# Kernel optimization log

Measured on AMD Instinct MI355X. Metric: run time of the kernel, lower is better.

The kernel has to match this reference:

```python
import jax, jax.numpy as jnp
import numpy as np

HID, NH, NKV, HD = 2048, 16, 8, 128
EPS = 1e-6
THETA = 10000.0
SCALE = HD ** -0.5


def setup_inputs() -> dict:
    key = jax.random.key(0)
    ks = jax.random.split(key, 6)
    S = 2048
    return {
        "positions": jnp.arange(S, dtype=jnp.int32),
        "hidden_states": jax.random.normal(ks[0], (S, HID), dtype=jnp.float32),
        "layernorm_weight": jax.random.uniform(ks[1], (HID,), dtype=jnp.float32, minval=0.5, maxval=1.5),
        "w_qkv": jax.random.normal(ks[2], ((NH + 2 * NKV) * HD, HID), dtype=jnp.float32) * 0.02,
        "w_o": jax.random.normal(ks[3], (HID, NH * HD), dtype=jnp.float32) * 0.02,
        "q_norm_w": jax.random.uniform(ks[4], (HD,), dtype=jnp.float32, minval=0.5, maxval=1.5),
        "k_norm_w": jax.random.uniform(ks[5], (HD,), dtype=jnp.float32, minval=0.5, maxval=1.5),
    }


def _rmsnorm(x, w, eps=EPS):
    var = jnp.mean(jnp.square(x), axis=-1, keepdims=True)
    return x * jax.lax.rsqrt(var + eps) * w


def _rope(x, cos, sin):
    # x: [S, h, HD]; cos/sin: [S, 1, HD//2] (neox-style rotate-half)
    x1, x2 = x[..., : HD // 2], x[..., HD // 2 :]
    return jnp.concatenate([x1 * cos - x2 * sin, x2 * cos + x1 * sin], axis=-1)


def reference(positions, hidden_states, layernorm_weight, w_qkv, w_o, q_norm_w, k_norm_w):
    S = hidden_states.shape[0]
    # Fused RMSNorm + QKV projection
    hn = _rmsnorm(hidden_states, layernorm_weight)
    qkv = hn @ w_qkv.T  # [S, (NH+2*NKV)*HD]
    q, k, v = jnp.split(qkv, [NH * HD, (NH + NKV) * HD], axis=-1)
    q = q.reshape(S, NH, HD)
    k = k.reshape(S, NKV, HD)
    v = v.reshape(S, NKV, HD)
    # Per-head QK RMSNorm
    q = _rmsnorm(q, q_norm_w)
    k = _rmsnorm(k, k_norm_w)
    # RoPE
    inv_freq = 1.0 / (THETA ** (jnp.arange(0, HD, 2, dtype=jnp.float32) / HD))
    freqs = positions.astype(jnp.float32)[:, None] * inv_freq  # [S, HD//2]
    cos = jnp.cos(freqs)[:, None, :]
    sin = jnp.sin(freqs)[:, None, :]
    q = _rope(q, cos, sin)
    k = _rope(k, cos, sin)
    # GQA: expand kv heads to match query heads
    rep = NH // NKV
    k = jnp.repeat(k, rep, axis=1)  # [S, NH, HD]
    v = jnp.repeat(v, rep, axis=1)
    # Causal attention
    scores = jnp.einsum("shd,thd->hst", q, k) * SCALE  # [NH, S, S]
    causal = jnp.tril(jnp.ones((S, S), dtype=bool))
    scores = jnp.where(causal, scores, jnp.finfo(scores.dtype).min)
    probs = jax.nn.softmax(scores, axis=-1)
    out = jnp.einsum("hst,thd->shd", probs, v)  # [S, NH, HD]
    # Output projection
    return out.reshape(S, NH * HD) @ w_o.T
```

## Files before the change

kernel.cpp:

```cpp
#include <hip/hip_runtime.h>
#include <hip/hip_bf16.h>
#include <math.h>

#define HID 2048
#define NH 16
#define NKV 8
#define HD 128
#define SEQ 2048
#define EPS 1e-6f
#define SCALE 0.08838834764831845f

typedef __attribute__((ext_vector_type(8))) short bf8_t;
typedef __attribute__((ext_vector_type(4))) float f4_t;

__device__ __forceinline__ short f2bf(float f) {
    union { __hip_bfloat16 h; short s; } u;
    u.h = __float2bfloat16(f);
    return u.s;
}
__device__ __forceinline__ float bf2f(short s) {
    union { short s; __hip_bfloat16 h; } u;
    u.s = s;
    return __bfloat162float(u.h);
}
__device__ __forceinline__ bf8_t pack8(const float4& a, const float4& b) {
    bf8_t r;
    r[0] = f2bf(a.x); r[1] = f2bf(a.y); r[2] = f2bf(a.z); r[3] = f2bf(a.w);
    r[4] = f2bf(b.x); r[5] = f2bf(b.y); r[6] = f2bf(b.z); r[7] = f2bf(b.w);
    return r;
}
__device__ __forceinline__ void gload16(const short* g, short* l) {
    __builtin_amdgcn_global_load_lds(
        (const __attribute__((address_space(1))) unsigned int*)g,
        (__attribute__((address_space(3))) unsigned int*)l, 16, 0, 0);
}

__device__ __forceinline__ float wave_reduce_sum(float v) {
#pragma unroll
    for (int off = 32; off > 0; off >>= 1) v += __shfl_xor(v, off);
    return v;
}

__global__ __launch_bounds__(256) void prep_kernel(
    const float* __restrict__ w_qkv, short* __restrict__ wqb,
    const float* __restrict__ w_o, short* __restrict__ wob,
    const float* __restrict__ x, const float* __restrict__ w,
    short* __restrict__ out) {
    int bid = blockIdx.x;
    int tid = threadIdx.x;
    if (bid < 4096) {
        int i = bid * 256 + tid;
        float4 a = *(const float4*)(w_qkv + (size_t)i * 8);
        float4 b = *(const float4*)(w_qkv + (size_t)i * 8 + 4);
        *(bf8_t*)(wqb + (size_t)i * 8) = pack8(a, b);
        return;
    }
    if (bid < 6144) {
        int i = (bid - 4096) * 256 + tid;
        float4 a = *(const float4*)(w_o + (size_t)i * 8);
        float4 b = *(const float4*)(w_o + (size_t)i * 8 + 4);
        *(bf8_t*)(wob + (size_t)i * 8) = pack8(a, b);
        return;
    }
    int row = bid - 6144;
    const float* xr = x + (size_t)row * HID;
    float4 a = *(const float4*)(xr + tid * 8);
    float4 b = *(const float4*)(xr + tid * 8 + 4);
    float ss = a.x * a.x + a.y * a.y + a.z * a.z + a.w * a.w +
               b.x * b.x + b.y * b.y + b.z * b.z + b.w * b.w;
    ss = wave_reduce_sum(ss);
    __shared__ float part[4];
    __shared__ float s_scale;
    if ((tid & 63) == 0) part[tid >> 6] = ss;
    __syncthreads();
    if (tid == 0) {
        float t = part[0] + part[1] + part[2] + part[3];
        s_scale = rsqrtf(t / (float)HID + EPS);
    }
    __syncthreads();
    float sc = s_scale;
    float4 wa = *(const float4*)(w + tid * 8);
    float4 wb = *(const float4*)(w + tid * 8 + 4);
    float4 oa = make_float4(a.x * sc * wa.x, a.y * sc * wa.y,
                            a.z * sc * wa.z, a.w * sc * wa.w);
    float4 ob = make_float4(b.x * sc * wb.x, b.y * sc * wb.y,
                            b.z * sc * wb.z, b.w * sc * wb.w);
    *(bf8_t*)(out + (size_t)row * HID + tid * 8) = pack8(oa, ob);
}

template <int MODE>
__global__ __launch_bounds__(256) void gemm_mfma_kernel(
    const short* __restrict__ A, const short* __restrict__ B,
    float* __restrict__ Cf, short* __restrict__ Q, short* __restrict__ Kp,
    short* __restrict__ Vr, int M, int N, int K) {
    __shared__ short As[128][64];
    __shared__ short Bs[128][64];
    int tid = threadIdx.x;
    int wv = tid >> 6, lane = tid & 63;
    int n16 = lane & 15, qd = lane >> 4;
    int m0 = blockIdx.y * 128, n0 = blockIdx.x * 128;
    int wm = (wv >> 1) * 64, wn = (wv & 1) * 64;
    int sr8 = lane >> 3, slot = lane & 7;

    size_t ainv[4], binv[4];
#pragma unroll
    for (int it = 0; it < 4; ++it) {
        int row = wv * 32 + it * 8 + sr8;
        int chunk = (slot - row) & 7;
        ainv[it] = (size_t)(m0 + row) * K + chunk * 8;
        binv[it] = (size_t)(n0 + row) * K + chunk * 8;
    }

    f4_t acc[4][4];
#pragma unroll
    for (int i = 0; i < 4; ++i)
#pragma unroll
        for (int j = 0; j < 4; ++j) acc[i][j] = (f4_t){0.f, 0.f, 0.f, 0.f};

    for (int k0 = 0; k0 < K; k0 += 64) {
        __syncthreads();
#pragma unroll
        for (int it = 0; it < 4; ++it) {
            gload16(A + ainv[it] + k0, &As[wv * 32 + it * 8][0]);
            gload16(B + binv[it] + k0, &Bs[wv * 32 + it * 8][0]);
        }
        __syncthreads();

        bf8_t af[4][2], bf[4][2];
#pragma unroll
        for (int t = 0; t < 4; ++t)
#pragma unroll
            for (int ks = 0; ks < 2; ++ks) {
                int ar = wm + t * 16 + n16;
                af[t][ks] = *(const bf8_t*)&As[ar][(((ks * 4 + qd) + ar) & 7) * 8];
                int br = wn + t * 16 + n16;
                bf[t][ks] = *(const bf8_t*)&Bs[br][(((ks * 4 + qd) + br) & 7) * 8];
            }
#pragma unroll
        for (int ks = 0; ks < 2; ++ks)
#pragma unroll
            for (int mt = 0; mt < 4; ++mt)
#pragma unroll
                for (int nt = 0; nt < 4; ++nt)
                    acc[mt][nt] = __builtin_amdgcn_mfma_f32_16x16x32_bf16(
                        af[mt][ks], bf[nt][ks], acc[mt][nt], 0, 0, 0);
    }

#pragma unroll
    for (int mt = 0; mt < 4; ++mt)
#pragma unroll
        for (int nt = 0; nt < 4; ++nt)
#pragma unroll
            for (int r = 0; r < 4; ++r) {
                int gm = m0 + wm + mt * 16 + qd * 4 + r;
                int gn = n0 + wn + nt * 16 + n16;
                float v = acc[mt][nt][r];
                if (MODE == 0) {
                    Cf[(size_t)gm * N + gn] = v;
                } else {
                    if (gn < NH * HD)
                        Q[(size_t)gm * (NH * HD) + gn] = f2bf(v);
                    else if (gn < (NH + NKV) * HD)
                        Kp[(size_t)gm * (NKV * HD) + (gn - NH * HD)] = f2bf(v);
                    else
                        Vr[(size_t)gm * (NKV * HD) + (gn - (NH + NKV) * HD)] = f2bf(v);
                }
            }
}

__global__ __launch_bounds__(256) void mid_kernel(
    const short* __restrict__ vr, short* __restrict__ vt,
    short* __restrict__ q, short* __restrict__ k,
    const float* __restrict__ qw, const float* __restrict__ kw,
    const int* __restrict__ pos) {
    int bid = blockIdx.x;
    int tid = threadIdx.x;
    if (bid < 512) {
        __shared__ short t[64][64];
        int s0 = (bid & 31) * 64, d0 = (bid >> 5) * 64;
        int sl = tid >> 3, ch = tid & 7;
#pragma unroll
        for (int it = 0; it < 2; ++it) {
            int s_local = it * 32 + sl;
            bf8_t vv = *(const bf8_t*)(vr + (size_t)(s0 + s_local) * (NKV * HD) + d0 + ch * 8);
            *(bf8_t*)&t[s_local][((ch + s_local) & 7) * 8] = vv;
        }
        __syncthreads();
#pragma unroll
        for (int it = 0; it < 2; ++it) {
            int d_local = it * 32 + sl;
            int sbase = ch * 8;
            bf8_t o;
#pragma unroll
            for (int j = 0; j < 8; ++j) {
                int s = sbase + j;
                o[j] = t[s][(((d_local >> 3) + s) & 7) * 8 + (d_local & 7)];
            }
            *(bf8_t*)(vt + (size_t)(d0 + d_local) * SEQ + s0 + sbase) = o;
        }
        return;
    }
    int u = (bid - 512) * 2 + (tid >> 7);
    int ui = tid >> 7, d = tid & 127;
    int s = u / 24, hh = u % 24;
    short* ptr;
    const float* w;
    if (hh < NH) {
        ptr = q + (size_t)s * (NH * HD) + hh * HD;
        w = qw;
    } else {
        ptr = k + (size_t)s * (NKV * HD) + (hh - NH) * HD;
        w = kw;
    }
    float x = bf2f(ptr[d]);
    float ss = wave_reduce_sum(x * x);
    __shared__ float part[2][2];
    if ((d & 63) == 0) part[ui][d >> 6] = ss;
    __syncthreads();
    float tot = part[ui][0] + part[ui][1];
    float xn = x * rsqrtf(tot / (float)HD + EPS) * w[d];
    __shared__ float sh[2][HD];
    sh[ui][d] = xn;
    __syncthreads();
    int j = d & 63;
    float inv = __expf((float)j * -0.14391156831f);
    float fr = (float)pos[s] * inv;
    float sn, cs;
    __sincosf(fr, &sn, &cs);
    float o;
    if (d < 64)
        o = xn * cs - sh[ui][d + 64] * sn;
    else
        o = xn * cs + sh[ui][d - 64] * sn;
    ptr[d] = f2bf(o);
}

__device__ __forceinline__ void attn_stage(
    short (&kb)[64][128], short (&vb)[128][64],
    const short* __restrict__ kg, const short* __restrict__ vg,
    int t0, const int (&kinv)[4], const int (&vinv)[4], int wv) {
#pragma unroll
    for (int it = 0; it < 4; ++it) {
        gload16(kg + (size_t)t0 * (NKV * HD) + kinv[it], &kb[wv * 16 + it * 4][0]);
        gload16(vg + t0 + vinv[it], &vb[wv * 32 + it * 8][0]);
    }
}

__device__ __forceinline__ void attn_tile(
    const short (&kb)[64][128], const short (&vb)[128][64],
    short (&psh)[4][2][16][64],
    const bf8_t (&qf)[2][4], f4_t (&of)[2][8],
    float (&m_i)[2][4], float (&l_p)[2][4],
    int wv, int n, int qd, int koff) {
    f4_t sc[2][4];
#pragma unroll
    for (int g = 0; g < 2; ++g)
#pragma unroll
        for (int kk = 0; kk < 4; ++kk) sc[g][kk] = (f4_t){0.f, 0.f, 0.f, 0.f};
#pragma unroll
    for (int kk = 0; kk < 4; ++kk) {
        int key = kk * 16 + n;
#pragma unroll
        for (int ks = 0; ks < 4; ++ks) {
            bf8_t kf = *(const bf8_t*)&kb[key][(((ks * 4 + qd) + key) & 15) * 8];
            sc[0][kk] = __builtin_amdgcn_mfma_f32_16x16x32_bf16(qf[0][ks], kf, sc[0][kk], 0, 0, 0);
            sc[1][kk] = __builtin_amdgcn_mfma_f32_16x16x32_bf16(qf[1][ks], kf, sc[1][kk], 0, 0, 0);
        }
    }
#pragma unroll
    for (int g = 0; g < 2; ++g) {
        int rows0 = wv * 32 + g * 16;
        bool needm = (koff + 63 > rows0);
#pragma unroll
        for (int kk = 0; kk < 4; ++kk)
#pragma unroll
            for (int r = 0; r < 4; ++r) {
                float s = sc[g][kk][r] * SCALE;
                if (needm && (koff + kk * 16 + n > rows0 + qd * 4 + r)) s = -1e30f;
                sc[g][kk][r] = s;
            }
#pragma unroll
        for (int r = 0; r < 4; ++r) {
            float mx = fmaxf(fmaxf(sc[g][0][r], sc[g][1][r]),
                             fmaxf(sc[g][2][r], sc[g][3][r]));
#pragma unroll
            for (int off = 1; off < 16; off <<= 1) mx = fmaxf(mx, __shfl_xor(mx, off));
            float mnew = fmaxf(m_i[g][r], mx);
            float al = __expf(m_i[g][r] - mnew);
            m_i[g][r] = mnew;
            float lsum = 0.f;
            int row = qd * 4 + r;
#pragma unroll
            for (int kk = 0; kk < 4; ++kk) {
                float p = __expf(sc[g][kk][r] - mnew);
                psh[wv][g][row][((kk * 16 + n) + row * 8) & 63] = f2bf(p);
                lsum += p;
            }
            l_p[g][r] = l_p[g][r] * al + lsum;
#pragma unroll
            for (int nb = 0; nb < 8; ++nb) of[g][nb][r] *= al;
        }
    }
    __builtin_amdgcn_wave_barrier();
#pragma unroll
    for (int ks2 = 0; ks2 < 2; ++ks2) {
        bf8_t pf0 = *(const bf8_t*)&psh[wv][0][n][((ks2 * 32 + qd * 8) + n * 8) & 63];
        bf8_t pf1 = *(const bf8_t*)&psh[wv][1][n][((ks2 * 32 + qd * 8) + n * 8) & 63];
#pragma unroll
        for (int nb = 0; nb < 8; ++nb) {
            int dim = nb * 16 + n;
            bf8_t vf = *(const bf8_t*)&vb[dim][(((ks2 * 4 + qd) + dim) & 7) * 8];
            of[0][nb] = __builtin_amdgcn_mfma_f32_16x16x32_bf16(pf0, vf, of[0][nb], 0, 0, 0);
            of[1][nb] = __builtin_amdgcn_mfma_f32_16x16x32_bf16(pf1, vf, of[1][nb], 0, 0, 0);
        }
    }
}

__global__ __launch_bounds__(256, 2) void attn_chunk_kernel(
    const short* __restrict__ q, const short* __restrict__ k,
    const short* __restrict__ vt, short* __restrict__ opart,
    float* __restrict__ ml) {
    __shared__ short kbufA[64][128], kbufB[64][128];
    __shared__ short vbufA[128][64], vbufB[128][64];
    __shared__ short psh[4][2][16][64];

    int tid = threadIdx.x;
    int wv = tid >> 6, lane = tid & 63;
    int n = lane & 15, qd = lane >> 4;

    int i = blockIdx.x;
    int hs = i >> 8, p = i & 255;
    int h = p >> 4;
    int qt = hs ? (p & 15) : (15 - (p & 15));
    int c = hs;
    int qbase = qt * 128;
    int tstart = c ? (qt + 1) : 0;
    int tcount = qt + 1;
    int kvh = h >> 1;

    int kinv[4], vinv[4];
#pragma unroll
    for (int it = 0; it < 4; ++it) {
        int key = wv * 16 + it * 4 + (lane >> 4);
        int ck = ((lane & 15) - key) & 15;
        kinv[it] = key * (NKV * HD) + kvh * HD + ck * 8;
        int dim = wv * 32 + it * 8 + (lane >> 3);
        int cv = ((lane & 7) - dim) & 7;
        vinv[it] = (kvh * HD + dim) * SEQ + cv * 8;
    }

    bf8_t qf[2][4];
#pragma unroll
    for (int g = 0; g < 2; ++g) {
        const short* qp =
            q + (size_t)(qbase + wv * 32 + g * 16 + n) * (NH * HD) + h * HD + qd * 8;
#pragma unroll
        for (int ks = 0; ks < 4; ++ks) qf[g][ks] = *(const bf8_t*)(qp + ks * 32);
    }

    f4_t of[2][8];
#pragma unroll
    for (int g = 0; g < 2; ++g)
#pragma unroll
        for (int x = 0; x < 8; ++x) of[g][x] = (f4_t){0.f, 0.f, 0.f, 0.f};
    float m_i[2][4] = {{-1e30f, -1e30f, -1e30f, -1e30f},
                       {-1e30f, -1e30f, -1e30f, -1e30f}};
    float l_p[2][4] = {{0.f, 0.f, 0.f, 0.f}, {0.f, 0.f, 0.f, 0.f}};

    attn_stage(kbufA, vbufA, k, vt, tstart * 64, kinv, vinv, wv);
    for (int tt = 0; tt < tcount; tt += 2) {
        __syncthreads();
        if (tt + 1 < tcount)
            attn_stage(kbufB, vbufB, k, vt, (tstart + tt + 1) * 64, kinv, vinv, wv);
        attn_tile(kbufA, vbufA, psh, qf, of, m_i, l_p, wv, n, qd,
                  (tstart + tt) * 64 - qbase);
        if (tt + 1 < tcount) {
            __syncthreads();
            if (tt + 2 < tcount)
                attn_stage(kbufA, vbufA, k, vt, (tstart + tt + 2) * 64, kinv, vinv, wv);
            attn_tile(kbufB, vbufB, psh, qf, of, m_i, l_p, wv, n, qd,
                      (tstart + tt + 1) * 64 - qbase);
        }
    }

    float lred[2][4];
#pragma unroll
    for (int g = 0; g < 2; ++g)
#pragma unroll
        for (int r = 0; r < 4; ++r) {
            float l = l_p[g][r];
#pragma unroll
            for (int off = 1; off < 16; off <<= 1) l += __shfl_xor(l, off);
            lred[g][r] = l;
        }

    size_t pb = ((size_t)(h * 16 + qt)) * 2 + c;
    short* op = opart + pb * (128 * 128);
#pragma unroll
    for (int g = 0; g < 2; ++g)
#pragma unroll
        for (int nb = 0; nb < 8; ++nb)
#pragma unroll
            for (int r = 0; r < 4; ++r) {
                int rl = wv * 32 + g * 16 + qd * 4 + r;
                op[rl * 128 + nb * 16 + n] = f2bf(of[g][nb][r]);
            }
    if (n == 0) {
#pragma unroll
        for (int g = 0; g < 2; ++g)
#pragma unroll
            for (int r = 0; r < 4; ++r) {
                int rl = wv * 32 + g * 16 + qd * 4 + r;
                ml[pb * 256 + rl * 2] = m_i[g][r];
                ml[pb * 256 + rl * 2 + 1] = lred[g][r];
            }
    }
}

__global__ __launch_bounds__(256) void attn_merge_kernel(
    const short* __restrict__ opart, const float* __restrict__ ml,
    short* __restrict__ o) {
    int bid = blockIdx.x;
    int h = bid >> 4, qt = bid & 15;
    int tid = threadIdx.x;
    int r = tid >> 1, hf = tid & 1;
    size_t pb0 = ((size_t)(h * 16 + qt)) * 2;
    size_t pb1 = pb0 + 1;
    float m0 = ml[pb0 * 256 + r * 2], l0 = ml[pb0 * 256 + r * 2 + 1];
    float m1 = ml[pb1 * 256 + r * 2], l1 = ml[pb1 * 256 + r * 2 + 1];
    float M = fmaxf(m0, m1);
    float w0 = __expf(m0 - M), w1 = __expf(m1 - M);
    float invL = 1.0f / (w0 * l0 + w1 * l1);
    int row = qt * 128 + r;
#pragma unroll
    for (int j = 0; j < 8; ++j) {
        int d0 = hf * 64 + j * 8;
        bf8_t a = *(const bf8_t*)(opart + pb0 * (128 * 128) + r * 128 + d0);
        bf8_t b = *(const bf8_t*)(opart + pb1 * (128 * 128) + r * 128 + d0);
        bf8_t e;
#pragma unroll
        for (int x = 0; x < 8; ++x)
            e[x] = f2bf((w0 * bf2f(a[x]) + w1 * bf2f(b[x])) * invL);
        *(bf8_t*)(o + (size_t)row * (NH * HD) + h * HD + d0) = e;
    }
}

extern "C" void kernel_launch(void* const* d_in, const int* in_sizes, int n_in,
                              void* d_out, int out_size, void* d_ws, size_t ws_size,
                              hipStream_t stream) {
    const int* positions   = (const int*)d_in[0];
    const float* hidden    = (const float*)d_in[1];
    const float* ln_w      = (const float*)d_in[2];
    const float* w_qkv     = (const float*)d_in[3];
    const float* w_o       = (const float*)d_in[4];
    const float* q_norm_w  = (const float*)d_in[5];
    const float* k_norm_w  = (const float*)d_in[6];
    float* out = (float*)d_out;

    char* base = (char*)d_ws;
    short* hnb   = (short*)(base);
    short* wqb   = (short*)(base + ((size_t)8 << 20));
    short* vtb   = (short*)(base + ((size_t)8 << 20));
    float* mlbuf = (float*)(base + ((size_t)12 << 20));
    short* wob   = (short*)(base + ((size_t)24 << 20));
    short* qbf   = (short*)(base + ((size_t)32 << 20));
    short* kbf   = (short*)(base + ((size_t)40 << 20));
    short* vrow  = (short*)(base + ((size_t)44 << 20));
    short* opart = (short*)d_out;

    prep_kernel<<<8192, 256, 0, stream>>>(w_qkv, wqb, w_o, wob, hidden, ln_w, hnb);
    gemm_mfma_kernel<1><<<dim3(32, 16), 256, 0, stream>>>(
        hnb, wqb, nullptr, qbf, kbf, vrow, SEQ, (NH + 2 * NKV) * HD, HID);
    mid_kernel<<<512 + 24576, 256, 0, stream>>>(
        vrow, vtb, qbf, kbf, q_norm_w, k_norm_w, positions);
    attn_chunk_kernel<<<512, 256, 0, stream>>>(qbf, kbf, vtb, opart, mlbuf);
    attn_merge_kernel<<<256, 256, 0, stream>>>(opart, mlbuf, hnb);
    gemm_mfma_kernel<0><<<dim3(16, 16), 256, 0, stream>>>(
        hnb, wob, out, nullptr, nullptr, nullptr, SEQ, NH * HD, HID);
}
```

Baseline: 279.3 us.

## Split attention into fixed six-tile KV chunks with variable-count merge

Attention work is now partitioned into chunks of at most six 64-key tiles per query tile, giving 816 blocks instead of 512 two-way splits, and the merge kernel combines a variable number of partials. Shared memory drops from double-buffered K/V to single buffers and the P staging buffer is halved so three blocks fit per CU. The goal is better load balance and occupancy across the causal triangle. In exchange it gives up the prefetch overlap of loads with compute, and it writes and reads more partial outputs in the merge.

```diff
diff --git a/kernel.cpp b/kernel.cpp
--- a/kernel.cpp
+++ b/kernel.cpp
@@ -235,6 +235,15 @@
     ptr[d] = f2bf(o);
 }
 
+__constant__ int c_qtb[17] = {0,1,2,3,5,7,9,12,15,18,22,26,30,35,40,45,51};
+
+__device__ __forceinline__ short* part_ptr(short* opA, short* opB, int pb) {
+    return pb < 512 ? opA + (size_t)pb * 16384 : opB + (size_t)(pb - 512) * 16384;
+}
+__device__ __forceinline__ const short* part_ptrc(const short* opA, const short* opB, int pb) {
+    return pb < 512 ? opA + (size_t)pb * 16384 : opB + (size_t)(pb - 512) * 16384;
+}
+
 __device__ __forceinline__ void attn_stage(
     short (&kb)[64][128], short (&vb)[128][64],
     const short* __restrict__ kg, const short* __restrict__ vg,
@@ -248,7 +257,7 @@
 
 __device__ __forceinline__ void attn_tile(
     const short (&kb)[64][128], const short (&vb)[128][64],
-    short (&psh)[4][2][16][64],
+    short (&psh)[4][16][64],
     const bf8_t (&qf)[2][4], f4_t (&of)[2][8],
     float (&m_i)[2][4], float (&l_p)[2][4],
     int wv, int n, int qd, int koff) {
@@ -267,6 +276,7 @@
             sc[1][kk] = __builtin_amdgcn_mfma_f32_16x16x32_bf16(qf[1][ks], kf, sc[1][kk], 0, 0, 0);
         }
     }
+    bf8_t pf[2][2];
 #pragma unroll
     for (int g = 0; g < 2; ++g) {
         int rows0 = wv * 32 + g * 16;
@@ -293,50 +303,53 @@
 #pragma unroll
             for (int kk = 0; kk < 4; ++kk) {
                 float p = __expf(sc[g][kk][r] - mnew);
-                psh[wv][g][row][((kk * 16 + n) + row * 8) & 63] = f2bf(p);
+                psh[wv][row][((kk * 16 + n) + row * 8) & 63] = f2bf(p);
                 lsum += p;
             }
             l_p[g][r] = l_p[g][r] * al + lsum;
 #pragma unroll
             for (int nb = 0; nb < 8; ++nb) of[g][nb][r] *= al;
         }
-    }
-    __builtin_amdgcn_wave_barrier();
-#pragma unroll
-    for (int ks2 = 0; ks2 < 2; ++ks2) {
-        bf8_t pf0 = *(const bf8_t*)&psh[wv][0][n][((ks2 * 32 + qd * 8) + n * 8) & 63];
-        bf8_t pf1 = *(const bf8_t*)&psh[wv][1][n][((ks2 * 32 + qd * 8) + n * 8) & 63];
+        __builtin_amdgcn_wave_barrier();
+#pragma unroll
+        for (int ks2 = 0; ks2 < 2; ++ks2)
+            pf[g][ks2] = *(const bf8_t*)&psh[wv][n][((ks2 * 32 + qd * 8) + n * 8) & 63];
+        __builtin_amdgcn_wave_barrier();
+    }
+#pragma unroll
+    for (int ks2 = 0; ks2 < 2; ++ks2)
 #pragma unroll
         for (int nb = 0; nb < 8; ++nb) {
             int dim = nb * 16 + n;
             bf8_t vf = *(const bf8_t*)&vb[dim][(((ks2 * 4 + qd) + dim) & 7) * 8];
-            of[0][nb] = __builtin_amdgcn_mfma_f32_16x16x32_bf16(pf0, vf, of[0][nb], 0, 0, 0);
-            of[1][nb] = __builtin_amdgcn_mfma_f32_16x16x32_bf16(pf1, vf, of[1][nb], 0, 0, 0);
-        }
-    }
-}
-
-__global__ __launch_bounds__(256, 2) void attn_chunk_kernel(
+            of[0][nb] = __builtin_amdgcn_mfma_f32_16x16x32_bf16(pf[0][ks2], vf, of[0][nb], 0, 0, 0);
+            of[1][nb] = __builtin_amdgcn_mfma_f32_16x16x32_bf16(pf[1][ks2], vf, of[1][nb], 0, 0, 0);
+        }
+}
+
+__global__ __launch_bounds__(256, 3) void attn_chunk_kernel(
     const short* __restrict__ q, const short* __restrict__ k,
-    const short* __restrict__ vt, short* __restrict__ opart,
-    float* __restrict__ ml) {
-    __shared__ short kbufA[64][128], kbufB[64][128];
-    __shared__ short vbufA[128][64], vbufB[128][64];
-    __shared__ short psh[4][2][16][64];
+    const short* __restrict__ vt, short* __restrict__ opA,
+    short* __restrict__ opB, float* __restrict__ ml) {
+    __shared__ short kbuf[64][128];
+    __shared__ short vbuf[128][64];
+    __shared__ short psh[4][16][64];
 
     int tid = threadIdx.x;
     int wv = tid >> 6, lane = tid & 63;
     int n = lane & 15, qd = lane >> 4;
 
-    int i = blockIdx.x;
-    int hs = i >> 8, p = i & 255;
-    int h = p >> 4;
-    int qt = hs ? (p & 15) : (15 - (p & 15));
-    int c = hs;
+    int b = blockIdx.x;
+    int l = b >> 4, h = b & 15;
+    int qt = 0;
+#pragma unroll
+    for (int t = 1; t < 16; ++t) qt = (l >= c_qtb[t]) ? t : qt;
+    int c = l - c_qtb[qt];
+    int ntk = 2 * (qt + 1);
+    int tstart = c * 6;
+    int tcount = min(6, ntk - tstart);
+    int kvh = h >> 1;
     int qbase = qt * 128;
-    int tstart = c ? (qt + 1) : 0;
-    int tcount = qt + 1;
-    int kvh = h >> 1;
 
     int kinv[4], vinv[4];
 #pragma unroll
@@ -367,20 +380,12 @@
                        {-1e30f, -1e30f, -1e30f, -1e30f}};
     float l_p[2][4] = {{0.f, 0.f, 0.f, 0.f}, {0.f, 0.f, 0.f, 0.f}};
 
-    attn_stage(kbufA, vbufA, k, vt, tstart * 64, kinv, vinv, wv);
-    for (int tt = 0; tt < tcount; tt += 2) {
+    for (int tt = 0; tt < tcount; ++tt) {
         __syncthreads();
-        if (tt + 1 < tcount)
-            attn_stage(kbufB, vbufB, k, vt, (tstart + tt + 1) * 64, kinv, vinv, wv);
-        attn_tile(kbufA, vbufA, psh, qf, of, m_i, l_p, wv, n, qd,
+        attn_stage(kbuf, vbuf, k, vt, (tstart + tt) * 64, kinv, vinv, wv);
+        __syncthreads();
+        attn_tile(kbuf, vbuf, psh, qf, of, m_i, l_p, wv, n, qd,
                   (tstart + tt) * 64 - qbase);
-        if (tt + 1 < tcount) {
-            __syncthreads();
-            if (tt + 2 < tcount)
-                attn_stage(kbufA, vbufA, k, vt, (tstart + tt + 2) * 64, kinv, vinv, wv);
-            attn_tile(kbufB, vbufB, psh, qf, of, m_i, l_p, wv, n, qd,
-                      (tstart + tt + 1) * 64 - qbase);
-        }
     }
 
     float lred[2][4];
@@ -388,14 +393,14 @@
     for (int g = 0; g < 2; ++g)
 #pragma unroll
         for (int r = 0; r < 4; ++r) {
-            float l = l_p[g][r];
-#pragma unroll
-            for (int off = 1; off < 16; off <<= 1) l += __shfl_xor(l, off);
-            lred[g][r] = l;
-        }
-
-    size_t pb = ((size_t)(h * 16 + qt)) * 2 + c;
-    short* op = opart + pb * (128 * 128);
+            float lr = l_p[g][r];
+#pragma unroll
+            for (int off = 1; off < 16; off <<= 1) lr += __shfl_xor(lr, off);
+            lred[g][r] = lr;
+        }
+
+    int pb = h * 51 + l;
+    short* op = part_ptr(opA, opB, pb);
 #pragma unroll
     for (int g = 0; g < 2; ++g)
 #pragma unroll
@@ -411,36 +416,47 @@
 #pragma unroll
             for (int r = 0; r < 4; ++r) {
                 int rl = wv * 32 + g * 16 + qd * 4 + r;
-                ml[pb * 256 + rl * 2] = m_i[g][r];
-                ml[pb * 256 + rl * 2 + 1] = lred[g][r];
+                ml[(size_t)pb * 256 + rl * 2] = m_i[g][r];
+                ml[(size_t)pb * 256 + rl * 2 + 1] = lred[g][r];
             }
     }
 }
 
 __global__ __launch_bounds__(256) void attn_merge_kernel(
-    const short* __restrict__ opart, const float* __restrict__ ml,
-    short* __restrict__ o) {
+    const short* __restrict__ opA, const short* __restrict__ opB,
+    const float* __restrict__ ml, short* __restrict__ o) {
     int bid = blockIdx.x;
     int h = bid >> 4, qt = bid & 15;
+    int base = h * 51 + c_qtb[qt];
+    int cnt = c_qtb[qt + 1] - c_qtb[qt];
     int tid = threadIdx.x;
     int r = tid >> 1, hf = tid & 1;
-    size_t pb0 = ((size_t)(h * 16 + qt)) * 2;
-    size_t pb1 = pb0 + 1;
-    float m0 = ml[pb0 * 256 + r * 2], l0 = ml[pb0 * 256 + r * 2 + 1];
-    float m1 = ml[pb1 * 256 + r * 2], l1 = ml[pb1 * 256 + r * 2 + 1];
-    float M = fmaxf(m0, m1);
-    float w0 = __expf(m0 - M), w1 = __expf(m1 - M);
-    float invL = 1.0f / (w0 * l0 + w1 * l1);
+    float m[6], w[6];
+    float M = -1e30f;
+    for (int c = 0; c < cnt; ++c) {
+        m[c] = ml[(size_t)(base + c) * 256 + r * 2];
+        M = fmaxf(M, m[c]);
+    }
+    float L = 0.f;
+    for (int c = 0; c < cnt; ++c) {
+        w[c] = __expf(m[c] - M);
+        L += w[c] * ml[(size_t)(base + c) * 256 + r * 2 + 1];
+    }
+    float invL = 1.0f / L;
     int row = qt * 128 + r;
 #pragma unroll
     for (int j = 0; j < 8; ++j) {
         int d0 = hf * 64 + j * 8;
-        bf8_t a = *(const bf8_t*)(opart + pb0 * (128 * 128) + r * 128 + d0);
-        bf8_t b = *(const bf8_t*)(opart + pb1 * (128 * 128) + r * 128 + d0);
+        float acc[8] = {0.f, 0.f, 0.f, 0.f, 0.f, 0.f, 0.f, 0.f};
+        for (int c = 0; c < cnt; ++c) {
+            const short* op = part_ptrc(opA, opB, base + c);
+            bf8_t a = *(const bf8_t*)(op + r * 128 + d0);
+#pragma unroll
+            for (int x = 0; x < 8; ++x) acc[x] += w[c] * bf2f(a[x]);
+        }
         bf8_t e;
 #pragma unroll
-        for (int x = 0; x < 8; ++x)
-            e[x] = f2bf((w0 * bf2f(a[x]) + w1 * bf2f(b[x])) * invL);
+        for (int x = 0; x < 8; ++x) e[x] = f2bf(acc[x] * invL);
         *(bf8_t*)(o + (size_t)row * (NH * HD) + h * HD + d0) = e;
     }
 }
@@ -461,20 +477,21 @@
     short* hnb   = (short*)(base);
     short* wqb   = (short*)(base + ((size_t)8 << 20));
     short* vtb   = (short*)(base + ((size_t)8 << 20));
-    float* mlbuf = (float*)(base + ((size_t)12 << 20));
+    short* opB   = (short*)(base + ((size_t)12 << 20));
+    float* mlbuf = (float*)(base + ((size_t)43 << 19));
     short* wob   = (short*)(base + ((size_t)24 << 20));
     short* qbf   = (short*)(base + ((size_t)32 << 20));
     short* kbf   = (short*)(base + ((size_t)40 << 20));
     short* vrow  = (short*)(base + ((size_t)44 << 20));
-    short* opart = (short*)d_out;
+    short* opA   = (short*)d_out;
 
     prep_kernel<<<8192, 256, 0, stream>>>(w_qkv, wqb, w_o, wob, hidden, ln_w, hnb);
     gemm_mfma_kernel<1><<<dim3(32, 16), 256, 0, stream>>>(
         hnb, wqb, nullptr, qbf, kbf, vrow, SEQ, (NH + 2 * NKV) * HD, HID);
     mid_kernel<<<512 + 24576, 256, 0, stream>>>(
         vrow, vtb, qbf, kbf, q_norm_w, k_norm_w, positions);
-    attn_chunk_kernel<<<512, 256, 0, stream>>>(qbf, kbf, vtb, opart, mlbuf);
-    attn_merge_kernel<<<256, 256, 0, stream>>>(opart, mlbuf, hnb);
+    attn_chunk_kernel<<<816, 256, 0, stream>>>(qbf, kbf, vtb, opA, opB, mlbuf);
+    attn_merge_kernel<<<256, 256, 0, stream>>>(opA, opB, mlbuf, hnb);
     gemm_mfma_kernel<0><<<dim3(16, 16), 256, 0, stream>>>(
         hnb, wob, out, nullptr, nullptr, nullptr, SEQ, NH * HD, HID);
 }
```

Measured after the change: 331.0 us. +18.5%, slower.
